# Performance work log

Hardware: AMD Instinct MI355X
Metric: run time of the kernel (lower is better)

Reference implementation:

```python
import jax, jax.numpy as jnp
import numpy as np
from jax import lax

H = 8          # num_heads
LAM = 4.0      # lambda_scale
POOL = 8       # pool_ratio (effective, N % POOL == 0)
NS_ITERS = 5
NS_EPS = 1e-4
WHITE_EPS = 1e-5


def _lap_kernel(x, y):
    # x: [B,H,n,D], y: [B,H,m,D] -> exp(-||x_i - y_j||_1 / LAM): [B,H,n,m]
    l1 = jnp.sum(jnp.abs(x[:, :, :, None, :] - y[:, :, None, :, :]), axis=-1)
    return jnp.exp(-l1 / LAM)


def setup_inputs() -> dict:
    key = jax.random.key(0)
    ks = jax.random.split(key, 8)
    B, N, C = 2, 1024, 512
    s = 0.05  # weight scale for realistic magnitudes
    return {
        "x": jax.random.normal(ks[0], (B, N, C), jnp.float32),
        "attention_mask": jnp.ones((B, N), jnp.float32),
        "qkv_w": jax.random.normal(ks[1], (3 * C, C), jnp.float32) * s,
        "qkv_b": jax.random.normal(ks[2], (3 * C,), jnp.float32) * s,
        "proj_w": jax.random.normal(ks[3], (C, C), jnp.float32) * s,
        "proj_b": jax.random.normal(ks[4], (C,), jnp.float32) * s,
        "dwc_w": jax.random.normal(ks[5], (C, 1, 3), jnp.float32) * s,
        "dwc_b": jax.random.normal(ks[6], (C,), jnp.float32) * s,
    }


def reference(x, attention_mask, qkv_w, qkv_b, proj_w, proj_b, dwc_w, dwc_b):
    B, N, C = x.shape
    D = C // H
    tm = attention_mask                      # [B,N]
    mh = tm[:, None, :, None]                # [B,1,N,1] broadcast over heads

    qkv = (x @ qkv_w.T + qkv_b).reshape(B, N, 3, H, D).transpose(2, 0, 3, 1, 4)
    q, k, v = qkv[0] * mh, qkv[1] * mh, qkv[2] * mh   # [B,H,N,D]

    # NOTE: faithful to source: raw reshape of [B,N,H*D] into [B,C,N]
    v_sp = v.transpose(0, 2, 1, 3).reshape(B, C, N)
    q_sp = q.transpose(0, 2, 1, 3).reshape(B, C, N)
    k_sp = k.transpose(0, 2, 1, 3).reshape(B, C, N)

    # depthwise conv1d, kernel 3, padding 1
    v_local = lax.conv_general_dilated(
        v_sp, dwc_w, window_strides=(1,), padding=[(1, 1)],
        feature_group_count=C, dimension_numbers=("NCH", "OIH", "NCH")
    ) + dwc_b[None, :, None]
    v_local = v_local.transpose(0, 2, 1) * tm[:, :, None]   # [B,N,C]

    p = POOL
    m = N // p
    pm = tm.reshape(B, 1, m, p).mean(-1)                    # [B,1,m]
    pms = jnp.clip(pm, 1e-6)
    q_pool = (q_sp * tm[:, None, :]).reshape(B, C, m, p).mean(-1) / pms
    k_pool = (k_sp * tm[:, None, :]).reshape(B, C, m, p).mean(-1) / pms
    lmask = (pm > 0).astype(x.dtype)[:, 0, :]               # [B,m]

    q_l = q_pool.transpose(0, 2, 1).reshape(B, m, H, D).transpose(0, 2, 1, 3)
    k_l = k_pool.transpose(0, 2, 1).reshape(B, m, H, D).transpose(0, 2, 1, 3)

    W = _lap_kernel(q_l, k_l)                               # [B,H,m,m]
    pair = lmask[:, None, :, None] * lmask[:, None, None, :]
    I = jnp.eye(m, dtype=x.dtype)[None, None]
    W = W * pair + I * (1.0 - pair)

    # Newton-Schulz pseudo-inverse
    W_eps = W + NS_EPS * I
    fro = jnp.sqrt(jnp.sum(W_eps * W_eps, axis=(-2, -1), keepdims=True))
    X = (2.0 / (fro + 1e-8)) * jnp.swapaxes(W_eps, -2, -1)
    for _ in range(NS_ITERS):
        X = X @ (2.0 * I - W_eps @ X)
    W_inv = X

    la_mask = lmask[:, None, None, :]                        # [B,1,1,m]
    C_q = _lap_kernel(q, k_l) * la_mask                      # [B,H,N,m]
    C_k = _lap_kernel(k, q_l) * la_mask                      # [B,H,N,m]

    # batch-statistics whitening of C_q over dims (0,2)
    qmask = tm[:, None, :, None]                             # [B,1,N,1]
    valid = jnp.clip(jnp.sum(qmask, axis=(0, 2), keepdims=True), 1.0)
    mu = jnp.sum(C_q * qmask, axis=(0, 2), keepdims=True) / valid
    cen = (C_q - mu) * qmask
    var = jnp.sum(cen * cen, axis=(0, 2), keepdims=True) / valid
    C_q_norm = ((C_q - mu) / jnp.sqrt(var + WHITE_EPS)) * qmask

    context = W_inv @ (jnp.swapaxes(C_k, -2, -1) @ v)        # [B,H,m,D]
    ga = (C_q_norm @ context) * mh                           # [B,H,N,D]
    ga = ga.transpose(0, 2, 1, 3).reshape(B, N, C)

    out = (ga + v_local) @ proj_w.T + proj_b
    return out * tm[:, :, None]
```

## Files before the change

### kernel.cpp

```cpp
#include <hip/hip_runtime.h>
#include <hip/hip_bf16.h>
#include <hip/hip_fp16.h>

#define Hh 8
#define Bz 2
#define Nn 1024
#define Cc 512
#define Dd 64
#define Mm 128
#define NS_EPS 1e-4f
#define WHITE_EPS 1e-5f

__device__ __forceinline__ float h2f(__half v) { return __half2float(v); }
__device__ __forceinline__ __half f2h(float v) { return __float2half(v); }

typedef _Float16 half8 __attribute__((ext_vector_type(8)));
typedef float float4v __attribute__((ext_vector_type(4)));

__global__ __launch_bounds__(256) void qkv_gemm(
    const float* __restrict__ x, const float* __restrict__ w,
    const float* __restrict__ bias, const float* __restrict__ tm,
    __half* __restrict__ Q, __half* __restrict__ K, __half* __restrict__ V) {
  __shared__ _Float16 As[128 * 40];
  __shared__ _Float16 Bs[128 * 40];
  int m0 = blockIdx.x * 128, n0 = blockIdx.y * 128;
  int tid = threadIdx.x;
  int lane = tid & 63, wv = tid >> 6;
  int wm = (wv >> 1) * 64, wn = (wv & 1) * 64;
  int l15 = lane & 15, quad = lane >> 4;
  int srow = tid >> 1, shalf = tid & 1;
  float4v acc[4][4] = {};
  for (int k0 = 0; k0 < 512; k0 += 32) {
    __syncthreads();
    {
      const float4* ga = (const float4*)(x + (size_t)(m0 + srow) * 512 + k0 + shalf * 16);
      const float4* gb = (const float4*)(w + (size_t)(n0 + srow) * 512 + k0 + shalf * 16);
      float4 a0 = ga[0], a1 = ga[1], a2 = ga[2], a3 = ga[3];
      float4 b0 = gb[0], b1 = gb[1], b2 = gb[2], b3 = gb[3];
      half8 ha0 = {(_Float16)a0.x, (_Float16)a0.y, (_Float16)a0.z, (_Float16)a0.w,
                   (_Float16)a1.x, (_Float16)a1.y, (_Float16)a1.z, (_Float16)a1.w};
      half8 ha1 = {(_Float16)a2.x, (_Float16)a2.y, (_Float16)a2.z, (_Float16)a2.w,
                   (_Float16)a3.x, (_Float16)a3.y, (_Float16)a3.z, (_Float16)a3.w};
      half8 hb0 = {(_Float16)b0.x, (_Float16)b0.y, (_Float16)b0.z, (_Float16)b0.w,
                   (_Float16)b1.x, (_Float16)b1.y, (_Float16)b1.z, (_Float16)b1.w};
      half8 hb1 = {(_Float16)b2.x, (_Float16)b2.y, (_Float16)b2.z, (_Float16)b2.w,
                   (_Float16)b3.x, (_Float16)b3.y, (_Float16)b3.z, (_Float16)b3.w};
      int lo = srow * 40 + shalf * 16;
      *(half8*)&As[lo] = ha0;
      *(half8*)&As[lo + 8] = ha1;
      *(half8*)&Bs[lo] = hb0;
      *(half8*)&Bs[lo + 8] = hb1;
    }
    __syncthreads();
    half8 a[4], b[4];
#pragma unroll
    for (int mt = 0; mt < 4; ++mt)
      a[mt] = *(const half8*)&As[(wm + mt * 16 + l15) * 40 + quad * 8];
#pragma unroll
    for (int nt = 0; nt < 4; ++nt)
      b[nt] = *(const half8*)&Bs[(wn + nt * 16 + l15) * 40 + quad * 8];
#pragma unroll
    for (int mt = 0; mt < 4; ++mt)
#pragma unroll
      for (int nt = 0; nt < 4; ++nt)
        acc[mt][nt] =
            __builtin_amdgcn_mfma_f32_16x16x32_f16(a[mt], b[nt], acc[mt][nt], 0, 0, 0);
  }
#pragma unroll
  for (int mt = 0; mt < 4; ++mt) {
#pragma unroll
    for (int r = 0; r < 4; ++r) {
      int row = m0 + wm + mt * 16 + quad * 4 + r;
      int b_ = row >> 10, n_ = row & 1023;
      float t = tm[b_ * 1024 + n_];
#pragma unroll
      for (int nt = 0; nt < 4; ++nt) {
        int c3 = n0 + wn + nt * 16 + l15;
        float v = (acc[mt][nt][r] + bias[c3]) * t;
        int sec = c3 >> 9, ch = c3 & 511;
        __half* dst = (sec == 0) ? Q : (sec == 1 ? K : V);
        dst[(size_t)b_ * (Nn * Cc) + (size_t)n_ * 512 + ch] = f2h(v);
      }
    }
  }
}

__global__ __launch_bounds__(256) void pool_kernel(
    const __half* __restrict__ Q, const __half* __restrict__ K,
    const float* __restrict__ tm, __half* __restrict__ QL,
    __half* __restrict__ KL, float* __restrict__ LM) {
  int ut = blockIdx.x;
  int bh = blockIdx.y;
  int b = bh >> 3, h = bh & 7;
  int u0 = ut * 64;
  int delta = u0 >> 9;
  int ch0 = u0 & 511;
  __shared__ float Qs[64][65];
  __shared__ float Ks[64][65];
  int tid = threadIdx.x;
  for (int e = tid; e < 4096; e += 256) {
    int d = e >> 6, uu = e & 63;
    int row = 2 * (h * 64 + d) + delta;
    size_t gi = (size_t)b * (Nn * Cc) + (size_t)row * 512 + ch0 + uu;
    Qs[d][uu] = h2f(Q[gi]);
    Ks[d][uu] = h2f(K[gi]);
  }
  __syncthreads();
  int d = tid & 63, s = tid >> 6;
#pragma unroll
  for (int jr = 0; jr < 2; ++jr) {
    int jl = s + 4 * jr;
    int j = ut * 8 + jl;
    float pm = 0.f, sq = 0.f, sk = 0.f;
#pragma unroll
    for (int i = 0; i < 8; ++i) {
      float t = tm[b * 1024 + 8 * j + i];
      pm += t;
      sq += Qs[d][8 * jl + i] * t;
      sk += Ks[d][8 * jl + i] * t;
    }
    pm *= 0.125f;
    float pms = fmaxf(pm, 1e-6f);
    size_t oi = ((size_t)bh * 128 + j) * 64 + d;
    QL[oi] = f2h(sq * 0.125f / pms);
    KL[oi] = f2h(sk * 0.125f / pms);
    if (h == 0 && d == 0) LM[b * 128 + j] = (pm > 0.f) ? 1.f : 0.f;
  }
}

__global__ __launch_bounds__(256) void fused_phase1(
    const __half* __restrict__ Q, const __half* __restrict__ K,
    const __half* __restrict__ V, const __half* __restrict__ QL,
    const __half* __restrict__ KL, const float* __restrict__ LM,
    const float* __restrict__ tm, __half* __restrict__ Wh,
    float* __restrict__ KTVp, float* __restrict__ PS,
    __half* __restrict__ Pbuf) {
  __shared__ __align__(16) char smem[47616];
  int id = blockIdx.x;
  int tid = threadIdx.x;
  if (id < 512) {
    int jt = id & 3, bh = (id >> 2) & 15, nc = id >> 6;
    int b = bh >> 3, h = bh & 7;
    int j0 = jt * 32;
    float* kls = (float*)smem;
    float* Qs = (float*)(smem + 8704);
    float* red = (float*)(smem + 17408);
    int sr = tid >> 3, sd8 = (tid & 7) * 8;
    {
      half8 q = *(const half8*)(KL + (size_t)bh * 8192 + (size_t)(j0 + sr) * 64 + sd8);
      float4 f0 = {(float)q[0], (float)q[1], (float)q[2], (float)q[3]};
      float4 f1 = {(float)q[4], (float)q[5], (float)q[6], (float)q[7]};
      *(float4*)&kls[sr * 68 + sd8] = f0;
      *(float4*)&kls[sr * 68 + sd8 + 4] = f1;
    }
    int jq = tid & 15, nq = tid >> 4;
    int jA = j0 + jq * 2, jB = jA + 1;
    float lmA = LM[b * 128 + jA], lmB = LM[b * 128 + jB];
    float aA1 = 0.f, aA2 = 0.f, aA3 = 0.f, aB1 = 0.f, aB2 = 0.f, aB3 = 0.f;
    for (int nt = 0; nt < 4; ++nt) {
      int n0 = nc * 128 + nt * 32;
      __syncthreads();
      {
        size_t gi = (size_t)b * (Nn * Cc) + (size_t)(n0 + sr) * 512 + h * 64 + sd8;
        half8 kv = *(const half8*)(Q + gi);
        float4 k0 = {(float)kv[0], (float)kv[1], (float)kv[2], (float)kv[3]};
        float4 k1 = {(float)kv[4], (float)kv[5], (float)kv[6], (float)kv[7]};
        *(float4*)&Qs[sr * 68 + sd8] = k0;
        *(float4*)&Qs[sr * 68 + sd8 + 4] = k1;
      }
      __syncthreads();
      const float4* q0p = (const float4*)&kls[(jq * 2) * 68];
      const float4* q1p = (const float4*)&kls[(jq * 2 + 1) * 68];
      const float4* k0p = (const float4*)&Qs[(nq * 2) * 68];
      const float4* k1p = (const float4*)&Qs[(nq * 2 + 1) * 68];
      float s00 = 0.f, s01 = 0.f, s10 = 0.f, s11 = 0.f;
#pragma unroll
      for (int i = 0; i < 16; ++i) {
        int dq = (i + tid) & 15;
        float4 q0 = q0p[dq], q1 = q1p[dq];
        float4 k0 = k0p[dq], k1 = k1p[dq];
        s00 += fabsf(q0.x - k0.x) + fabsf(q0.y - k0.y) + fabsf(q0.z - k0.z) + fabsf(q0.w - k0.w);
        s01 += fabsf(q0.x - k1.x) + fabsf(q0.y - k1.y) + fabsf(q0.z - k1.z) + fabsf(q0.w - k1.w);
        s10 += fabsf(q1.x - k0.x) + fabsf(q1.y - k0.y) + fabsf(q1.z - k0.z) + fabsf(q1.w - k0.w);
        s11 += fabsf(q1.x - k1.x) + fabsf(q1.y - k1.y) + fabsf(q1.z - k1.z) + fabsf(q1.w - k1.w);
      }
      int nA = n0 + nq * 2, nB = nA + 1;
      float tA = tm[b * 1024 + nA], tB = tm[b * 1024 + nB];
      float xAa = expf(-s00 * 0.25f) * lmA;
      float xAb = expf(-s01 * 0.25f) * lmA;
      float xBa = expf(-s10 * 0.25f) * lmB;
      float xBb = expf(-s11 * 0.25f) * lmB;
      Pbuf[((size_t)bh * 1024 + nA) * 128 + jA] = f2h(xAa);
      Pbuf[((size_t)bh * 1024 + nB) * 128 + jA] = f2h(xAb);
      Pbuf[((size_t)bh * 1024 + nA) * 128 + jB] = f2h(xBa);
      Pbuf[((size_t)bh * 1024 + nB) * 128 + jB] = f2h(xBb);
      float xt;
      xt = xAa * tA; aA1 += xt; aA2 += xt * xt; aA3 += xt * tA;
      xt = xAb * tB; aA1 += xt; aA2 += xt * xt; aA3 += xt * tB;
      xt = xBa * tA; aB1 += xt; aB2 += xt * xt; aB3 += xt * tA;
      xt = xBb * tB; aB1 += xt; aB2 += xt * xt; aB3 += xt * tB;
    }
    int jl = jq * 2;
    red[(jl * 8 + nq) * 3 + 0] = aA1;
    red[(jl * 8 + nq) * 3 + 1] = aA2;
    red[(jl * 8 + nq) * 3 + 2] = aA3;
    red[((jl + 1) * 8 + nq) * 3 + 0] = aB1;
    red[((jl + 1) * 8 + nq) * 3 + 1] = aB2;
    red[((jl + 1) * 8 + nq) * 3 + 2] = aB3;
    __syncthreads();
    if (tid < 32) {
      float s1 = 0.f, s2 = 0.f, s3 = 0.f;
#pragma unroll
      for (int q = 0; q < 8; ++q) {
        s1 += red[(tid * 8 + q) * 3 + 0];
        s2 += red[(tid * 8 + q) * 3 + 1];
        s3 += red[(tid * 8 + q) * 3 + 2];
      }
      size_t base = ((size_t)(nc * 16 + bh) * 128 + j0 + tid) * 3;
      PS[base] = s1; PS[base + 1] = s2; PS[base + 2] = s3;
    }
  } else if (id < 768) {
    int kid = id - 512;
    int jt = kid & 3, bh = (kid >> 2) & 15, nc = kid >> 6;
    int b = bh >> 3, h = bh & 7;
    int j0 = jt * 32;
    float* qls = (float*)smem;
    float* Ks = (float*)(smem + 8704);
    float* Vs = (float*)(smem + 17408);
    float* P = (float*)(smem + 26112);
    int sr = tid >> 3, sd8 = (tid & 7) * 8;
    {
      half8 q = *(const half8*)(QL + (size_t)bh * 8192 + (size_t)(j0 + sr) * 64 + sd8);
      float4 f0 = {(float)q[0], (float)q[1], (float)q[2], (float)q[3]};
      float4 f1 = {(float)q[4], (float)q[5], (float)q[6], (float)q[7]};
      *(float4*)&qls[sr * 68 + sd8] = f0;
      *(float4*)&qls[sr * 68 + sd8 + 4] = f1;
    }
    int jq = tid & 15, nq = tid >> 4;
    int dq2 = tid & 7, jl = tid >> 3;
    float acc[8] = {};
    for (int nt = 0; nt < 8; ++nt) {
      int n0 = nc * 256 + nt * 32;
      __syncthreads();
      {
        size_t gi = (size_t)b * (Nn * Cc) + (size_t)(n0 + sr) * 512 + h * 64 + sd8;
        half8 kv = *(const half8*)(K + gi);
        half8 vv = *(const half8*)(V + gi);
        float4 k0 = {(float)kv[0], (float)kv[1], (float)kv[2], (float)kv[3]};
        float4 k1 = {(float)kv[4], (float)kv[5], (float)kv[6], (float)kv[7]};
        float4 v0 = {(float)vv[0], (float)vv[1], (float)vv[2], (float)vv[3]};
        float4 v1 = {(float)vv[4], (float)vv[5], (float)vv[6], (float)vv[7]};
        *(float4*)&Ks[sr * 68 + sd8] = k0;
        *(float4*)&Ks[sr * 68 + sd8 + 4] = k1;
        *(float4*)&Vs[sr * 68 + sd8] = v0;
        *(float4*)&Vs[sr * 68 + sd8 + 4] = v1;
      }
      __syncthreads();
      {
        const float4* q0p = (const float4*)&qls[(jq * 2) * 68];
        const float4* q1p = (const float4*)&qls[(jq * 2 + 1) * 68];
        const float4* k0p = (const float4*)&Ks[(nq * 2) * 68];
        const float4* k1p = (const float4*)&Ks[(nq * 2 + 1) * 68];
        float s00 = 0.f, s01 = 0.f, s10 = 0.f, s11 = 0.f;
#pragma unroll
        for (int i = 0; i < 16; ++i) {
          int dq = (i + tid) & 15;
          float4 q0 = q0p[dq], q1 = q1p[dq];
          float4 k0 = k0p[dq], k1 = k1p[dq];
          s00 += fabsf(q0.x - k0.x) + fabsf(q0.y - k0.y) + fabsf(q0.z - k0.z) + fabsf(q0.w - k0.w);
          s01 += fabsf(q0.x - k1.x) + fabsf(q0.y - k1.y) + fabsf(q0.z - k1.z) + fabsf(q0.w - k1.w);
          s10 += fabsf(q1.x - k0.x) + fabsf(q1.y - k0.y) + fabsf(q1.z - k0.z) + fabsf(q1.w - k0.w);
          s11 += fabsf(q1.x - k1.x) + fabsf(q1.y - k1.y) + fabsf(q1.z - k1.z) + fabsf(q1.w - k1.w);
        }
        P[(nq * 2) * 36 + jq * 2] = expf(-s00 * 0.25f);
        P[(nq * 2) * 36 + jq * 2 + 1] = expf(-s10 * 0.25f);
        P[(nq * 2 + 1) * 36 + jq * 2] = expf(-s01 * 0.25f);
        P[(nq * 2 + 1) * 36 + jq * 2 + 1] = expf(-s11 * 0.25f);
      }
      __syncthreads();
      {
#pragma unroll 4
        for (int n = 0; n < 32; ++n) {
          float p = P[n * 36 + jl];
          float4 v0 = *(const float4*)&Vs[n * 68 + dq2 * 8];
          float4 v1 = *(const float4*)&Vs[n * 68 + dq2 * 8 + 4];
          acc[0] += p * v0.x; acc[1] += p * v0.y; acc[2] += p * v0.z; acc[3] += p * v0.w;
          acc[4] += p * v1.x; acc[5] += p * v1.y; acc[6] += p * v1.z; acc[7] += p * v1.w;
        }
      }
    }
    {
      float lm = LM[b * 128 + j0 + jl];
      float* dst = &KTVp[((size_t)nc * 16 + bh) * 8192 + (size_t)(j0 + jl) * 64 + dq2 * 8];
      float4 o0 = {acc[0] * lm, acc[1] * lm, acc[2] * lm, acc[3] * lm};
      float4 o1 = {acc[4] * lm, acc[5] * lm, acc[6] * lm, acc[7] * lm};
      *(float4*)dst = o0;
      *(float4*)(dst + 4) = o1;
    }
  } else {
    int wid = id - 768;
    int it = wid >> 4, bh = wid & 15;
    int b = bh >> 3;
    int i0 = it * 16;
    float* kls = (float*)smem;
    float* qs = (float*)(smem + 34816);
    float* ps = (float*)(smem + 39168);
    for (int e = tid; e < 8192; e += 256)
      kls[(e >> 6) * 68 + (e & 63)] = h2f(KL[(size_t)bh * 8192 + e]);
    for (int e = tid; e < 1024; e += 256)
      qs[(e >> 6) * 68 + (e & 63)] =
          h2f(QL[(size_t)bh * 8192 + (size_t)(i0 + (e >> 6)) * 64 + (e & 63)]);
    __syncthreads();
    int jg = tid & 63, ng = tid >> 6;
    int j = jg * 2;
    const float4* kA = (const float4*)&kls[j * 68];
    const float4* kB = (const float4*)&kls[(j + 1) * 68];
    float sA[4] = {}, sB[4] = {};
#pragma unroll
    for (int i = 0; i < 16; ++i) {
      int dq = (i + jg) & 15;
      float4 ka = kA[dq];
      float4 kb = kB[dq];
#pragma unroll
      for (int r = 0; r < 4; ++r) {
        float4 qv = *(const float4*)&qs[(ng * 4 + r) * 68 + dq * 4];
        sA[r] += fabsf(qv.x - ka.x) + fabsf(qv.y - ka.y) + fabsf(qv.z - ka.z) + fabsf(qv.w - ka.w);
        sB[r] += fabsf(qv.x - kb.x) + fabsf(qv.y - kb.y) + fabsf(qv.z - kb.z) + fabsf(qv.w - kb.w);
      }
    }
    float lmA = LM[b * Mm + j], lmB = LM[b * Mm + j + 1];
#pragma unroll
    for (int r = 0; r < 4; ++r) {
      int i = i0 + ng * 4 + r;
      float lmi = LM[b * Mm + i];
      float prA = lmi * lmA, prB = lmi * lmB;
      float dA = (i == j) ? 1.f : 0.f;
      float dB = (i == j + 1) ? 1.f : 0.f;
      ps[(ng * 4 + r) * 132 + j] = expf(-sA[r] * 0.25f) * prA + dA * (1.f - prA) + dA * NS_EPS;
      ps[(ng * 4 + r) * 132 + j + 1] = expf(-sB[r] * 0.25f) * prB + dB * (1.f - prB) + dB * NS_EPS;
    }
    __syncthreads();
    for (int e = tid; e < 2048; e += 256)
      Wh[(size_t)bh * (Mm * Mm) + (size_t)(i0 + (e >> 7)) * 128 + (e & 127)] =
          f2h(ps[(e >> 7) * 132 + (e & 127)]);
  }
}

__global__ __launch_bounds__(1024) void fused_phase2(
    const __half* __restrict__ Wh, const float* __restrict__ KTVp,
    const float* __restrict__ PS, const float* __restrict__ tm,
    __half* __restrict__ CTX, float* __restrict__ MU, float* __restrict__ RS) {
  __shared__ __align__(16) char smem[143360];
  int tid = threadIdx.x;
  if (blockIdx.x < 16) {
    int bh = blockIdx.x;
    _Float16* Ws = (_Float16*)smem;
    _Float16* Xa = (_Float16*)(smem + 34816);
    _Float16* Xb = (_Float16*)(smem + 69632);
    _Float16* Tt = (_Float16*)(smem + 104448);
    float* red = (float*)(smem + 139264);
    const __half* Wb = Wh + (size_t)bh * 16384;
    float fro = 0.f;
    for (int e = tid; e < 16384; e += 1024) {
      float wv = h2f(Wb[e]);
      Ws[(e >> 7) * 136 + (e & 127)] = (_Float16)wv;
      fro += wv * wv;
    }
    red[tid] = fro;
    __syncthreads();
    for (int off = 512; off > 0; off >>= 1) {
      if (tid < off) red[tid] += red[tid + off];
      __syncthreads();
    }
    float scale = 2.f / (sqrtf(red[0]) + 1e-8f);
    for (int e = tid; e < 16384; e += 1024) {
      int i = e >> 7, k = e & 127;
      Xa[i * 136 + k] = (_Float16)(scale * (float)Ws[k * 136 + i]);
      Xb[i * 136 + k] = (_Float16)(scale * (float)Ws[i * 136 + k]);
    }
    __syncthreads();
    int lane = tid & 63, wv_ = tid >> 6;
    int wm = (wv_ >> 2) * 32, wn = (wv_ & 3) * 32;
    int l15 = lane & 15, quad = lane >> 4;
    for (int it = 0; it < 5; ++it) {
      {
        float4v acc[2][2] = {};
#pragma unroll
        for (int kt = 0; kt < 4; ++kt) {
          half8 a[2], b[2];
#pragma unroll
          for (int mt = 0; mt < 2; ++mt)
            a[mt] = *(const half8*)&Ws[(wm + mt * 16 + l15) * 136 + kt * 32 + quad * 8];
#pragma unroll
          for (int nt = 0; nt < 2; ++nt)
            b[nt] = *(const half8*)&Xb[(wn + nt * 16 + l15) * 136 + kt * 32 + quad * 8];
#pragma unroll
          for (int mt = 0; mt < 2; ++mt)
#pragma unroll
            for (int nt = 0; nt < 2; ++nt)
              acc[mt][nt] =
                  __builtin_amdgcn_mfma_f32_16x16x32_f16(a[mt], b[nt], acc[mt][nt], 0, 0, 0);
        }
#pragma unroll
        for (int mt = 0; mt < 2; ++mt)
#pragma unroll
          for (int r = 0; r < 4; ++r) {
            int i = wm + mt * 16 + quad * 4 + r;
#pragma unroll
            for (int nt = 0; nt < 2; ++nt) {
              int j = wn + nt * 16 + l15;
              Tt[j * 136 + i] = (_Float16)(((i == j) ? 2.f : 0.f) - acc[mt][nt][r]);
            }
          }
      }
      __syncthreads();
      {
        float4v acc[2][2] = {};
#pragma unroll
        for (int kt = 0; kt < 4; ++kt) {
          half8 a[2], b[2];
#pragma unroll
          for (int mt = 0; mt < 2; ++mt)
            a[mt] = *(const half8*)&Xa[(wm + mt * 16 + l15) * 136 + kt * 32 + quad * 8];
#pragma unroll
          for (int nt = 0; nt < 2; ++nt)
            b[nt] = *(const half8*)&Tt[(wn + nt * 16 + l15) * 136 + kt * 32 + quad * 8];
#pragma unroll
          for (int mt = 0; mt < 2; ++mt)
#pragma unroll
            for (int nt = 0; nt < 2; ++nt)
              acc[mt][nt] =
                  __builtin_amdgcn_mfma_f32_16x16x32_f16(a[mt], b[nt], acc[mt][nt], 0, 0, 0);
        }
        __syncthreads();
#pragma unroll
        for (int mt = 0; mt < 2; ++mt)
#pragma unroll
          for (int r = 0; r < 4; ++r) {
            int i = wm + mt * 16 + quad * 4 + r;
#pragma unroll
            for (int nt = 0; nt < 2; ++nt) {
              int j = wn + nt * 16 + l15;
              _Float16 v = (_Float16)acc[mt][nt][r];
              Xa[i * 136 + j] = v;
              Xb[j * 136 + i] = v;
            }
          }
      }
      __syncthreads();
    }
    float* KTVs = (float*)smem;
    for (int e = tid; e < 8192; e += 1024) {
      float s = KTVp[(size_t)bh * 8192 + e];
#pragma unroll
      for (int nc = 1; nc < 4; ++nc) s += KTVp[((size_t)nc * 16 + bh) * 8192 + e];
      KTVs[(e >> 6) * 68 + (e & 63)] = s;
    }
    __syncthreads();
    int i = tid >> 3, d0 = (tid & 7) * 8;
    float a0 = 0.f, a1 = 0.f, a2 = 0.f, a3 = 0.f;
    float a4 = 0.f, a5 = 0.f, a6 = 0.f, a7 = 0.f;
#pragma unroll 4
    for (int j = 0; j < 128; ++j) {
      float xv = (float)Xa[i * 136 + j];
      float4 k0 = *(const float4*)&KTVs[j * 68 + d0];
      float4 k1 = *(const float4*)&KTVs[j * 68 + d0 + 4];
      a0 += xv * k0.x; a1 += xv * k0.y; a2 += xv * k0.z; a3 += xv * k0.w;
      a4 += xv * k1.x; a5 += xv * k1.y; a6 += xv * k1.z; a7 += xv * k1.w;
    }
    half8 hout = {(_Float16)a0, (_Float16)a1, (_Float16)a2, (_Float16)a3,
                  (_Float16)a4, (_Float16)a5, (_Float16)a6, (_Float16)a7};
    *(half8*)(CTX + (size_t)bh * 8192 + (size_t)i * 64 + d0) = hout;
  } else {
    float (*red2)[2] = (float(*)[2])smem;
    float* ts = (float*)(smem + 8192);
    float a = 0.f, c = 0.f;
    for (int i = tid; i < 2048; i += 1024) { float t = tm[i]; a += t; c += t * t; }
    red2[tid][0] = a; red2[tid][1] = c;
    __syncthreads();
    for (int off = 512; off > 0; off >>= 1) {
      if (tid < off) { red2[tid][0] += red2[tid + off][0]; red2[tid][1] += red2[tid + off][1]; }
      __syncthreads();
    }
    if (tid == 0) { ts[0] = red2[0][0]; ts[1] = red2[0][1]; }
    __syncthreads();
    int hj = tid;
    int h = hj >> 7, j = hj & 127;
    float s1 = 0.f, s2 = 0.f, s3 = 0.f;
#pragma unroll
    for (int nc = 0; nc < 8; ++nc)
#pragma unroll
      for (int b = 0; b < 2; ++b) {
        const float* p = PS + ((size_t)(nc * 16 + b * 8 + h) * 128 + j) * 3;
        s1 += p[0]; s2 += p[1]; s3 += p[2];
      }
    float valid = fmaxf(ts[0], 1.f);
    float mu = s1 / valid;
    float var = (s2 - 2.f * mu * s3 + mu * mu * ts[1]) / valid;
    var = fmaxf(var, 0.f);
    MU[hj] = mu;
    RS[hj] = rsqrtf(var + WHITE_EPS);
  }
}

__global__ __launch_bounds__(256) void ga_fused(
    const __half* __restrict__ Pbuf, const float* __restrict__ MU,
    const float* __restrict__ RS, const __half* __restrict__ CTXg,
    const __half* __restrict__ V, const float* __restrict__ dwc_w,
    const float* __restrict__ dwc_b, const float* __restrict__ tm,
    __half* __restrict__ VL) {
  int bh = blockIdx.y;
  int b = bh >> 3, h = bh & 7;
  int n0 = blockIdx.x * 16;
  __shared__ __half Ps[16][130];
  __shared__ __align__(16) __half2 ctx2[128][32];
  __shared__ float musr[128][2];
  int tid = threadIdx.x;
  for (int e = tid; e < 2048; e += 256)
    Ps[e >> 7][e & 127] = Pbuf[((size_t)bh * 1024 + n0 + (e >> 7)) * 128 + (e & 127)];
  {
    const __half2* cg = (const __half2*)(CTXg + (size_t)bh * 8192);
    for (int e = tid; e < 4096; e += 256) ctx2[e >> 5][e & 31] = cg[e];
  }
  if (tid < 128) { musr[tid][0] = MU[h * 128 + tid]; musr[tid][1] = RS[h * 128 + tid]; }
  __syncthreads();
  int nn = tid >> 4, dq = tid & 15;
  float a0 = 0.f, a1 = 0.f, a2 = 0.f, a3 = 0.f;
#pragma unroll 4
  for (int j = 0; j < 128; ++j) {
    float pj = (h2f(Ps[nn][j]) - musr[j][0]) * musr[j][1];
    uint2 cc = *(const uint2*)&ctx2[j][dq * 2];
    __half2 c01 = __builtin_bit_cast(__half2, cc.x);
    __half2 c23 = __builtin_bit_cast(__half2, cc.y);
    a0 += pj * h2f(c01.x); a1 += pj * h2f(c01.y);
    a2 += pj * h2f(c23.x); a3 += pj * h2f(c23.y);
  }
  int t = n0 + nn;
  float tmv = tm[b * 1024 + t];
  float t2 = tmv * tmv;
  float acc[4] = {a0 * t2, a1 * t2, a2 * t2, a3 * t2};
#pragma unroll
  for (int q = 0; q < 4; ++q) {
    int c = h * 64 + dq * 4 + q;
    float vacc = dwc_b[c];
#pragma unroll
    for (int k = 0; k < 3; ++k) {
      int u = t - 1 + k;
      if (u >= 0 && u < 1024) {
        int n = 2 * c + (u >> 9), ch = u & 511;
        vacc += dwc_w[c * 3 + k] * h2f(V[(size_t)b * (Nn * Cc) + (size_t)n * 512 + ch]);
      }
    }
    acc[q] += vacc * tmv;
  }
  size_t base = (size_t)b * (Nn * Cc) + (size_t)t * 512 + h * 64 + dq * 4;
  VL[base] = f2h(acc[0]);
  VL[base + 1] = f2h(acc[1]);
  VL[base + 2] = f2h(acc[2]);
  VL[base + 3] = f2h(acc[3]);
}

__global__ __launch_bounds__(256) void proj_gemm(
    const __half* __restrict__ Ain, const float* __restrict__ w,
    const float* __restrict__ bias, const float* __restrict__ tm,
    float* __restrict__ out) {
  __shared__ _Float16 As[128 * 40];
  __shared__ _Float16 Bs[128 * 40];
  int m0 = blockIdx.x * 128, n0 = blockIdx.y * 128;
  int tid = threadIdx.x;
  int lane = tid & 63, wv = tid >> 6;
  int wm = (wv >> 1) * 64, wn = (wv & 1) * 64;
  int l15 = lane & 15, quad = lane >> 4;
  int srow = tid >> 1, shalf = tid & 1;
  float4v acc[4][4] = {};
  for (int k0 = 0; k0 < 512; k0 += 32) {
    __syncthreads();
    {
      const half8* ga = (const half8*)(Ain + (size_t)(m0 + srow) * 512 + k0 + shalf * 16);
      const float4* gb = (const float4*)(w + (size_t)(n0 + srow) * 512 + k0 + shalf * 16);
      half8 ha0 = ga[0], ha1 = ga[1];
      float4 b0 = gb[0], b1 = gb[1], b2 = gb[2], b3 = gb[3];
      half8 hb0 = {(_Float16)b0.x, (_Float16)b0.y, (_Float16)b0.z, (_Float16)b0.w,
                   (_Float16)b1.x, (_Float16)b1.y, (_Float16)b1.z, (_Float16)b1.w};
      half8 hb1 = {(_Float16)b2.x, (_Float16)b2.y, (_Float16)b2.z, (_Float16)b2.w,
                   (_Float16)b3.x, (_Float16)b3.y, (_Float16)b3.z, (_Float16)b3.w};
      int lo = srow * 40 + shalf * 16;
      *(half8*)&As[lo] = ha0;
      *(half8*)&As[lo + 8] = ha1;
      *(half8*)&Bs[lo] = hb0;
      *(half8*)&Bs[lo + 8] = hb1;
    }
    __syncthreads();
    half8 a[4], b[4];
#pragma unroll
    for (int mt = 0; mt < 4; ++mt)
      a[mt] = *(const half8*)&As[(wm + mt * 16 + l15) * 40 + quad * 8];
#pragma unroll
    for (int nt = 0; nt < 4; ++nt)
      b[nt] = *(const half8*)&Bs[(wn + nt * 16 + l15) * 40 + quad * 8];
#pragma unroll
    for (int mt = 0; mt < 4; ++mt)
#pragma unroll
      for (int nt = 0; nt < 4; ++nt)
        acc[mt][nt] =
            __builtin_amdgcn_mfma_f32_16x16x32_f16(a[mt], b[nt], acc[mt][nt], 0, 0, 0);
  }
#pragma unroll
  for (int mt = 0; mt < 4; ++mt) {
#pragma unroll
    for (int r = 0; r < 4; ++r) {
      int row = m0 + wm + mt * 16 + quad * 4 + r;
      int b_ = row >> 10, n_ = row & 1023;
      float t = tm[b_ * 1024 + n_];
#pragma unroll
      for (int nt = 0; nt < 4; ++nt) {
        int co = n0 + wn + nt * 16 + l15;
        out[(size_t)row * 512 + co] = (acc[mt][nt][r] + bias[co]) * t;
      }
    }
  }
}

extern "C" void kernel_launch(void* const* d_in, const int* in_sizes, int n_in,
                              void* d_out, int out_size, void* d_ws, size_t ws_size,
                              hipStream_t stream) {
  const float* x      = (const float*)d_in[0];
  const float* tm     = (const float*)d_in[1];
  const float* qkv_w  = (const float*)d_in[2];
  const float* qkv_b  = (const float*)d_in[3];
  const float* proj_w = (const float*)d_in[4];
  const float* proj_b = (const float*)d_in[5];
  const float* dwc_w  = (const float*)d_in[6];
  const float* dwc_b  = (const float*)d_in[7];
  float* out = (float*)d_out;

  char* wsb = (char*)d_ws;
  __half* Qh  = (__half*)(wsb + 0);
  __half* Kh  = (__half*)(wsb + 2097152);
  __half* Vh  = (__half*)(wsb + 4194304);
  __half* VLh = (__half*)(wsb + 6291456);
  float*  KTVp = (float*)(wsb + 6291456);
  __half* QLh = (__half*)(wsb + 8388608);
  __half* KLh = (__half*)(wsb + 8650752);
  float*  LM  = (float*)(wsb + 8912896);
  float*  MU  = (float*)(wsb + 8913920);
  float*  RS  = (float*)(wsb + 8918016);
  __half* CTX = (__half*)(wsb + 8922112);
  float*  PS  = (float*)(wsb + 9184256);
  __half* Wh  = (__half*)(wsb + 9380864);

  __half* Pbuf = (__half*)d_out;

  qkv_gemm<<<dim3(16, 12), 256, 0, stream>>>(x, qkv_w, qkv_b, tm, Qh, Kh, Vh);
  pool_kernel<<<dim3(16, 16), 256, 0, stream>>>(Qh, Kh, tm, QLh, KLh, LM);
  fused_phase1<<<896, 256, 0, stream>>>(Qh, Kh, Vh, QLh, KLh, LM, tm, Wh, KTVp,
                                        PS, Pbuf);
  fused_phase2<<<17, 1024, 0, stream>>>(Wh, KTVp, PS, tm, CTX, MU, RS);
  ga_fused<<<dim3(64, 16), 256, 0, stream>>>(Pbuf, MU, RS, CTX, Vh, dwc_w, dwc_b, tm, VLh);
  proj_gemm<<<dim3(16, 4), 256, 0, stream>>>(VLh, proj_w, proj_b, tm, out);
}
```

Baseline: 207.2 us.

## Use exp2 intrinsic for Laplacian kernel, retile ga_fused and proj_gemm

Replaces expf(-s/4) with a hardware exp2 intrinsic on a prescaled argument in all three Laplacian-kernel sites. ga_fused now handles 64 rows per block with 4 rows per thread, reusing each context load across rows. proj_gemm moves from 128x128 to 64x64 tiles, giving 256 blocks instead of 64 so more CUs are busy. The exp2 path gives up a little accuracy, and the smaller GEMM tiles reuse less data per block.

Result: faster. 202.3 us (-2.4%).

```diff
diff --git a/kernel.cpp b/kernel.cpp
--- a/kernel.cpp
+++ b/kernel.cpp
@@ -10,9 +10,13 @@
 #define Mm 128
 #define NS_EPS 1e-4f
 #define WHITE_EPS 1e-5f
+#define NEG_L2E_OVER_LAM (-0.3606737602222409f)
 
 __device__ __forceinline__ float h2f(__half v) { return __half2float(v); }
 __device__ __forceinline__ __half f2h(float v) { return __float2half(v); }
+__device__ __forceinline__ float lapexp(float s) {
+  return __builtin_amdgcn_exp2f(s * NEG_L2E_OVER_LAM);
+}
 
 typedef _Float16 half8 __attribute__((ext_vector_type(8)));
 typedef float float4v __attribute__((ext_vector_type(4)));
@@ -186,10 +190,10 @@
       }
       int nA = n0 + nq * 2, nB = nA + 1;
       float tA = tm[b * 1024 + nA], tB = tm[b * 1024 + nB];
-      float xAa = expf(-s00 * 0.25f) * lmA;
-      float xAb = expf(-s01 * 0.25f) * lmA;
-      float xBa = expf(-s10 * 0.25f) * lmB;
-      float xBb = expf(-s11 * 0.25f) * lmB;
+      float xAa = lapexp(s00) * lmA;
+      float xAb = lapexp(s01) * lmA;
+      float xBa = lapexp(s10) * lmB;
+      float xBb = lapexp(s11) * lmB;
       Pbuf[((size_t)bh * 1024 + nA) * 128 + jA] = f2h(xAa);
       Pbuf[((size_t)bh * 1024 + nB) * 128 + jA] = f2h(xAb);
       Pbuf[((size_t)bh * 1024 + nA) * 128 + jB] = f2h(xBa);
@@ -272,10 +276,10 @@
           s10 += fabsf(q1.x - k0.x) + fabsf(q1.y - k0.y) + fabsf(q1.z - k0.z) + fabsf(q1.w - k0.w);
           s11 += fabsf(q1.x - k1.x) + fabsf(q1.y - k1.y) + fabsf(q1.z - k1.z) + fabsf(q1.w - k1.w);
         }
-        P[(nq * 2) * 36 + jq * 2] = expf(-s00 * 0.25f);
-        P[(nq * 2) * 36 + jq * 2 + 1] = expf(-s10 * 0.25f);
-        P[(nq * 2 + 1) * 36 + jq * 2] = expf(-s01 * 0.25f);
-        P[(nq * 2 + 1) * 36 + jq * 2 + 1] = expf(-s11 * 0.25f);
+        P[(nq * 2) * 36 + jq * 2] = lapexp(s00);
+        P[(nq * 2) * 36 + jq * 2 + 1] = lapexp(s10);
+        P[(nq * 2 + 1) * 36 + jq * 2] = lapexp(s01);
+        P[(nq * 2 + 1) * 36 + jq * 2 + 1] = lapexp(s11);
       }
       __syncthreads();
       {
@@ -336,8 +340,8 @@
       float prA = lmi * lmA, prB = lmi * lmB;
       float dA = (i == j) ? 1.f : 0.f;
       float dB = (i == j + 1) ? 1.f : 0.f;
-      ps[(ng * 4 + r) * 132 + j] = expf(-sA[r] * 0.25f) * prA + dA * (1.f - prA) + dA * NS_EPS;
-      ps[(ng * 4 + r) * 132 + j + 1] = expf(-sB[r] * 0.25f) * prB + dB * (1.f - prB) + dB * NS_EPS;
+      ps[(ng * 4 + r) * 132 + j] = lapexp(sA[r]) * prA + dA * (1.f - prA) + dA * NS_EPS;
+      ps[(ng * 4 + r) * 132 + j + 1] = lapexp(sB[r]) * prB + dB * (1.f - prB) + dB * NS_EPS;
     }
     __syncthreads();
     for (int e = tid; e < 2048; e += 256)
@@ -511,12 +515,12 @@
     __half* __restrict__ VL) {
   int bh = blockIdx.y;
   int b = bh >> 3, h = bh & 7;
-  int n0 = blockIdx.x * 16;
-  __shared__ __half Ps[16][130];
+  int n0 = blockIdx.x * 64;
+  __shared__ __half Ps[64][130];
   __shared__ __align__(16) __half2 ctx2[128][32];
   __shared__ float musr[128][2];
   int tid = threadIdx.x;
-  for (int e = tid; e < 2048; e += 256)
+  for (int e = tid; e < 8192; e += 256)
     Ps[e >> 7][e & 127] = Pbuf[((size_t)bh * 1024 + n0 + (e >> 7)) * 128 + (e & 127)];
   {
     const __half2* cg = (const __half2*)(CTXg + (size_t)bh * 8192);
@@ -525,95 +529,98 @@
   if (tid < 128) { musr[tid][0] = MU[h * 128 + tid]; musr[tid][1] = RS[h * 128 + tid]; }
   __syncthreads();
   int nn = tid >> 4, dq = tid & 15;
-  float a0 = 0.f, a1 = 0.f, a2 = 0.f, a3 = 0.f;
-#pragma unroll 4
+  float acc[4][4] = {};
+#pragma unroll 2
   for (int j = 0; j < 128; ++j) {
-    float pj = (h2f(Ps[nn][j]) - musr[j][0]) * musr[j][1];
+    float mu = musr[j][0], rs = musr[j][1];
     uint2 cc = *(const uint2*)&ctx2[j][dq * 2];
     __half2 c01 = __builtin_bit_cast(__half2, cc.x);
     __half2 c23 = __builtin_bit_cast(__half2, cc.y);
-    a0 += pj * h2f(c01.x); a1 += pj * h2f(c01.y);
-    a2 += pj * h2f(c23.x); a3 += pj * h2f(c23.y);
-  }
-  int t = n0 + nn;
-  float tmv = tm[b * 1024 + t];
-  float t2 = tmv * tmv;
-  float acc[4] = {a0 * t2, a1 * t2, a2 * t2, a3 * t2};
-#pragma unroll
-  for (int q = 0; q < 4; ++q) {
-    int c = h * 64 + dq * 4 + q;
-    float vacc = dwc_b[c];
-#pragma unroll
-    for (int k = 0; k < 3; ++k) {
-      int u = t - 1 + k;
-      if (u >= 0 && u < 1024) {
-        int n = 2 * c + (u >> 9), ch = u & 511;
-        vacc += dwc_w[c * 3 + k] * h2f(V[(size_t)b * (Nn * Cc) + (size_t)n * 512 + ch]);
-      }
-    }
-    acc[q] += vacc * tmv;
-  }
-  size_t base = (size_t)b * (Nn * Cc) + (size_t)t * 512 + h * 64 + dq * 4;
-  VL[base] = f2h(acc[0]);
-  VL[base + 1] = f2h(acc[1]);
-  VL[base + 2] = f2h(acc[2]);
-  VL[base + 3] = f2h(acc[3]);
+    float c0 = h2f(c01.x), c1 = h2f(c01.y), c2 = h2f(c23.x), c3 = h2f(c23.y);
+#pragma unroll
+    for (int rr = 0; rr < 4; ++rr) {
+      float pj = (h2f(Ps[nn + rr * 16][j]) - mu) * rs;
+      acc[rr][0] += pj * c0; acc[rr][1] += pj * c1;
+      acc[rr][2] += pj * c2; acc[rr][3] += pj * c3;
+    }
+  }
+#pragma unroll
+  for (int rr = 0; rr < 4; ++rr) {
+    int t = n0 + nn + rr * 16;
+    float tmv = tm[b * 1024 + t];
+    float t2 = tmv * tmv;
+    float o[4] = {acc[rr][0] * t2, acc[rr][1] * t2, acc[rr][2] * t2, acc[rr][3] * t2};
+#pragma unroll
+    for (int q = 0; q < 4; ++q) {
+      int c = h * 64 + dq * 4 + q;
+      float vacc = dwc_b[c];
+#pragma unroll
+      for (int k = 0; k < 3; ++k) {
+        int u = t - 1 + k;
+        if (u >= 0 && u < 1024) {
+          int n = 2 * c + (u >> 9), ch = u & 511;
+          vacc += dwc_w[c * 3 + k] * h2f(V[(size_t)b * (Nn * Cc) + (size_t)n * 512 + ch]);
+        }
+      }
+      o[q] += vacc * tmv;
+    }
+    size_t base = (size_t)b * (Nn * Cc) + (size_t)t * 512 + h * 64 + dq * 4;
+    VL[base] = f2h(o[0]);
+    VL[base + 1] = f2h(o[1]);
+    VL[base + 2] = f2h(o[2]);
+    VL[base + 3] = f2h(o[3]);
+  }
 }
 
 __global__ __launch_bounds__(256) void proj_gemm(
     const __half* __restrict__ Ain, const float* __restrict__ w,
     const float* __restrict__ bias, const float* __restrict__ tm,
     float* __restrict__ out) {
-  __shared__ _Float16 As[128 * 40];
-  __shared__ _Float16 Bs[128 * 40];
-  int m0 = blockIdx.x * 128, n0 = blockIdx.y * 128;
+  __shared__ _Float16 As[64 * 40];
+  __shared__ _Float16 Bs[64 * 40];
+  int m0 = blockIdx.x * 64, n0 = blockIdx.y * 64;
   int tid = threadIdx.x;
   int lane = tid & 63, wv = tid >> 6;
-  int wm = (wv >> 1) * 64, wn = (wv & 1) * 64;
+  int wm = (wv >> 1) * 32, wn = (wv & 1) * 32;
   int l15 = lane & 15, quad = lane >> 4;
-  int srow = tid >> 1, shalf = tid & 1;
-  float4v acc[4][4] = {};
+  int srow = tid >> 2, scol = (tid & 3) * 8;
+  float4v acc[2][2] = {};
   for (int k0 = 0; k0 < 512; k0 += 32) {
     __syncthreads();
     {
-      const half8* ga = (const half8*)(Ain + (size_t)(m0 + srow) * 512 + k0 + shalf * 16);
-      const float4* gb = (const float4*)(w + (size_t)(n0 + srow) * 512 + k0 + shalf * 16);
-      half8 ha0 = ga[0], ha1 = ga[1];
-      float4 b0 = gb[0], b1 = gb[1], b2 = gb[2], b3 = gb[3];
-      half8 hb0 = {(_Float16)b0.x, (_Float16)b0.y, (_Float16)b0.z, (_Float16)b0.w,
-                   (_Float16)b1.x, (_Float16)b1.y, (_Float16)b1.z, (_Float16)b1.w};
-      half8 hb1 = {(_Float16)b2.x, (_Float16)b2.y, (_Float16)b2.z, (_Float16)b2.w,
-                   (_Float16)b3.x, (_Float16)b3.y, (_Float16)b3.z, (_Float16)b3.w};
-      int lo = srow * 40 + shalf * 16;
-      *(half8*)&As[lo] = ha0;
-      *(half8*)&As[lo + 8] = ha1;
-      *(half8*)&Bs[lo] = hb0;
-      *(half8*)&Bs[lo + 8] = hb1;
-    }
-    __syncthreads();
-    half8 a[4], b[4];
-#pragma unroll
-    for (int mt = 0; mt < 4; ++mt)
+      half8 ha = *(const half8*)(Ain + (size_t)(m0 + srow) * 512 + k0 + scol);
+      const float4* gb = (const float4*)(w + (size_t)(n0 + srow) * 512 + k0 + scol);
+      float4 b0 = gb[0], b1 = gb[1];
+      half8 hb = {(_Float16)b0.x, (_Float16)b0.y, (_Float16)b0.z, (_Float16)b0.w,
+                  (_Float16)b1.x, (_Float16)b1.y, (_Float16)b1.z, (_Float16)b1.w};
+      int lo = srow * 40 + scol;
+      *(half8*)&As[lo] = ha;
+      *(half8*)&Bs[lo] = hb;
+    }
+    __syncthreads();
+    half8 a[2], b[2];
+#pragma unroll
+    for (int mt = 0; mt < 2; ++mt)
       a[mt] = *(const half8*)&As[(wm + mt * 16 + l15) * 40 + quad * 8];
 #pragma unroll
-    for (int nt = 0; nt < 4; ++nt)
+    for (int nt = 0; nt < 2; ++nt)
       b[nt] = *(const half8*)&Bs[(wn + nt * 16 + l15) * 40 + quad * 8];
 #pragma unroll
-    for (int mt = 0; mt < 4; ++mt)
-#pragma unroll
-      for (int nt = 0; nt < 4; ++nt)
+    for (int mt = 0; mt < 2; ++mt)
+#pragma unroll
+      for (int nt = 0; nt < 2; ++nt)
         acc[mt][nt] =
             __builtin_amdgcn_mfma_f32_16x16x32_f16(a[mt], b[nt], acc[mt][nt], 0, 0, 0);
   }
 #pragma unroll
-  for (int mt = 0; mt < 4; ++mt) {
+  for (int mt = 0; mt < 2; ++mt) {
 #pragma unroll
     for (int r = 0; r < 4; ++r) {
       int row = m0 + wm + mt * 16 + quad * 4 + r;
       int b_ = row >> 10, n_ = row & 1023;
       float t = tm[b_ * 1024 + n_];
 #pragma unroll
-      for (int nt = 0; nt < 4; ++nt) {
+      for (int nt = 0; nt < 2; ++nt) {
         int co = n0 + wn + nt * 16 + l15;
         out[(size_t)row * 512 + co] = (acc[mt][nt][r] + bias[co]) * t;
       }
@@ -656,6 +663,6 @@
   fused_phase1<<<896, 256, 0, stream>>>(Qh, Kh, Vh, QLh, KLh, LM, tm, Wh, KTVp,
                                         PS, Pbuf);
   fused_phase2<<<17, 1024, 0, stream>>>(Wh, KTVp, PS, tm, CTX, MU, RS);
-  ga_fused<<<dim3(64, 16), 256, 0, stream>>>(Pbuf, MU, RS, CTX, Vh, dwc_w, dwc_b, tm, VLh);
-  proj_gemm<<<dim3(16, 4), 256, 0, stream>>>(VLh, proj_w, proj_b, tm, out);
-}
+  ga_fused<<<dim3(16, 16), 256, 0, stream>>>(Pbuf, MU, RS, CTX, Vh, dwc_w, dwc_b, tm, VLh);
+  proj_gemm<<<dim3(32, 8), 256, 0, stream>>>(VLh, proj_w, proj_b, tm, out);
+}
```
